# Kernel tuning notes

Hardware: AMD Instinct MI355X
Metric: run time of the kernel (lower is better)

The kernel has to match this reference:

```python
import jax, jax.numpy as jnp
import numpy as np

DIM = 128
N = 4096


def setup_inputs() -> dict:
    key = jax.random.key(0)
    ks = jax.random.split(key, 12)
    d = DIM
    s = 0.02
    inp = jax.random.normal(ks[0], (N, 2 * d), dtype=jnp.float32)
    # H = myLinear: (2d -> 5d -> 1), tanh after each layer
    Hw1 = jax.random.normal(ks[1], (2 * d, 5 * d), dtype=jnp.float32) * s
    Hb1 = jax.random.normal(ks[2], (5 * d,), dtype=jnp.float32) * s
    Hw2 = jax.random.normal(ks[3], (5 * d, 1), dtype=jnp.float32) * s
    Hb2 = jax.random.normal(ks[4], (1,), dtype=jnp.float32) * s
    # augment_f: (d -> 4d -> 8d -> d*d), tanh after each layer
    Aw1 = jax.random.normal(ks[5], (d, 4 * d), dtype=jnp.float32) * s
    Ab1 = jax.random.normal(ks[6], (4 * d,), dtype=jnp.float32) * s
    Aw2 = jax.random.normal(ks[7], (4 * d, 8 * d), dtype=jnp.float32) * s
    Ab2 = jax.random.normal(ks[8], (8 * d,), dtype=jnp.float32) * s
    Aw3 = jax.random.normal(ks[9], (8 * d, d * d), dtype=jnp.float32) * s
    Ab3 = jax.random.normal(ks[10], (d * d,), dtype=jnp.float32) * s
    u = jax.random.uniform(ks[11], (d,), dtype=jnp.float32, minval=-0.001, maxval=0.001)
    return {"t": 0, "inp": inp, "Hw1": Hw1, "Hb1": Hb1, "Hw2": Hw2, "Hb2": Hb2,
            "Aw1": Aw1, "Ab1": Ab1, "Aw2": Aw2, "Ab2": Ab2, "Aw3": Aw3, "Ab3": Ab3, "u": u}


def reference(t, inp, Hw1, Hb1, Hw2, Hb2, Aw1, Ab1, Aw2, Ab2, Aw3, Ab3, u):
    d = DIM
    n = inp.shape[0]

    def H_scalar(z):  # z: [2d] -> scalar
        h = jnp.tanh(z @ Hw1 + Hb1)
        return jnp.tanh(h @ Hw2 + Hb2)[0]

    # per-sample gradient of scalar H w.r.t. input (== batch_jacobian squeeze)
    g = jax.vmap(jax.grad(H_scalar))(inp)  # [N, 2d]
    dx = g[:, :d]
    dv = -g[:, d:]

    x = inp[:, :d]
    h1 = jnp.tanh(x @ Aw1 + Ab1)            # [N, 4d]
    h2 = jnp.tanh(h1 @ Aw2 + Ab2)           # [N, 8d]
    gq = jnp.tanh(h2 @ Aw3 + Ab3).reshape(n, d, d)  # [N, d, d]
    dv = dv + jnp.einsum("nij,j->ni", gq, u)
    return jnp.concatenate([dx, dv], axis=-1)  # [N, 2d]
```

## Files before the change

kernel.cpp:

```cpp
#include <hip/hip_runtime.h>
#include <hip/hip_bf16.h>
#include <cstdint>


typedef __bf16 bf16_t;
typedef __bf16 bf16x4_t __attribute__((ext_vector_type(4)));
typedef __bf16 bf16x8_t __attribute__((ext_vector_type(8)));
typedef float f32x4_t __attribute__((ext_vector_type(4)));
typedef float f32x16_t __attribute__((ext_vector_type(16)));
typedef int intx4_t __attribute__((ext_vector_type(4)));
typedef int intx8_t __attribute__((ext_vector_type(8)));

#define DIMD 128
#define NROW 4096
#define SMEM_G64 24576
#define SMEM3_BYTES 32768

__device__ __forceinline__ float fast_tanh(float x) {
  float t = __builtin_amdgcn_exp2f(x * 2.8853900817779268f);
  return 1.f - 2.f * __builtin_amdgcn_rcpf(t + 1.f);
}

__device__ __forceinline__ uint8_t to_fp8(float x) {
  return (uint8_t)(__builtin_amdgcn_cvt_pk_fp8_f32(x, x, 0, false) & 0xff);
}

__device__ __forceinline__ uint32_t pk4_fp8(float a, float b, float c,
                                            float d) {
  uint32_t lo = (uint32_t)__builtin_amdgcn_cvt_pk_fp8_f32(a, b, 0, false);
  return (uint32_t)__builtin_amdgcn_cvt_pk_fp8_f32(c, d, lo, true);
}

__device__ __forceinline__ void g2l16(const void* gp, void* lp) {
  __builtin_amdgcn_global_load_lds(
      reinterpret_cast<__attribute__((address_space(1))) void*>(
          reinterpret_cast<uintptr_t>(gp)),
      reinterpret_cast<__attribute__((address_space(3))) void*>(
          reinterpret_cast<uintptr_t>(lp)),
      16, 0, 0);
}

template <int CTRL>
__device__ __forceinline__ float dpp_addf(float v) {
  return v + __int_as_float(__builtin_amdgcn_update_dpp(
                 0, __float_as_int(v), CTRL, 0xf, 0xf, true));
}
__device__ __forceinline__ float dpp_sum32(float v) {
  v = dpp_addf<0x111>(v);
  v = dpp_addf<0x112>(v);
  v = dpp_addf<0x114>(v);
  v = dpp_addf<0x118>(v);
  v = dpp_addf<0x142>(v);
  return v;
}

template <int EPI>
__device__ __forceinline__ void gemm64_body(char* smem, int bx, int by,
                                            const bf16_t* A, int lda,
                                            const bf16_t* B, int ldb, int K,
                                            const float* bias, void* outp,
                                            int ldo) {
  constexpr int BK = 32;
  bf16_t* As = (bf16_t*)smem;
  bf16_t* Bs = As + 3 * 2048;
  const int NT = K / BK;

  const int m0 = bx * 64;
  const int n0 = by * 64;
  const int tid = threadIdx.x;
  const int wave = tid >> 6;
  const int lane = tid & 63;
  const int wm = wave >> 1;
  const int wn = wave & 1;

  const int sr = lane >> 2;
  const int sk = (((lane & 3) ^ ((sr >> 1) & 3)) * 8);
  const int fr = lane & 15;
  const int fk = (((lane >> 4) ^ ((fr >> 1) & 3)) * 8);
  const int rb = wave * 16;

  const bf16_t* Ag = A + (size_t)(m0 + rb + sr) * lda + sk;
  const bf16_t* Bg = B + (size_t)(n0 + rb + sr) * ldb + sk;

#define G64_STAGE(buf, k0)                              \
  do {                                                  \
    g2l16(Ag + (k0), As + (buf) * 2048 + rb * BK);      \
    g2l16(Bg + (k0), Bs + (buf) * 2048 + rb * BK);      \
  } while (0)

  f32x4_t acc[2][2] = {};

  G64_STAGE(0, 0);
  G64_STAGE(1, BK);
  asm volatile("s_waitcnt vmcnt(2)" ::: "memory");
  __builtin_amdgcn_s_barrier();
  asm volatile("" ::: "memory");

  for (int t = 0; t < NT; ++t) {
    if (t + 2 < NT) G64_STAGE((t + 2) % 3, (t + 2) * BK);
    const bf16_t* Ab = As + (t % 3) * 2048;
    const bf16_t* Bb = Bs + (t % 3) * 2048;

    bf16x8_t af[2], bb[2];
#pragma unroll
    for (int u = 0; u < 2; ++u) {
      af[u] = *(const bf16x8_t*)(Ab + (wm * 32 + u * 16 + fr) * BK + fk);
      bb[u] = *(const bf16x8_t*)(Bb + (wn * 32 + u * 16 + fr) * BK + fk);
    }
#pragma unroll
    for (int i = 0; i < 2; ++i)
#pragma unroll
      for (int j = 0; j < 2; ++j)
        acc[i][j] = __builtin_amdgcn_mfma_f32_16x16x32_bf16(af[i], bb[j],
                                                            acc[i][j], 0, 0, 0);
    if (t < NT - 1) {
      if (t + 2 < NT)
        asm volatile("s_waitcnt vmcnt(2)" ::: "memory");
      else
        asm volatile("s_waitcnt vmcnt(0)" ::: "memory");
      __builtin_amdgcn_s_barrier();
      asm volatile("" ::: "memory");
    }
  }
#undef G64_STAGE

#pragma unroll
  for (int i = 0; i < 2; ++i) {
    const int row = m0 + wm * 32 + i * 16 + (lane >> 4) * 4;
#pragma unroll
    for (int j = 0; j < 2; ++j) {
      const int col = n0 + wn * 32 + j * 16 + fr;
      if constexpr (EPI == 0) {
        bf16_t* O = (bf16_t*)outp;
        const float b = bias[col];
#pragma unroll
        for (int r = 0; r < 4; ++r)
          O[(size_t)(row + r) * ldo + col] = (bf16_t)fast_tanh(acc[i][j][r] + b);
      } else if constexpr (EPI == 1) {
        float* O = (float*)outp;
        const bool dx = (n0 < DIMD);
#pragma unroll
        for (int r = 0; r < 4; ++r) {
          const size_t idx = (size_t)(row + r) * ldo + col;
          if (dx) O[idx] = acc[i][j][r];
          else atomicAdd(&O[idx], -acc[i][j][r]);
        }
      } else {
        uint8_t* O = (uint8_t*)outp;
        const float b = bias[col];
#pragma unroll
        for (int r = 0; r < 4; ++r)
          O[(size_t)(row + r) * ldo + col] =
              to_fp8(64.f * fast_tanh(acc[i][j][r] + b));
      }
    }
  }
}

__device__ __forceinline__ void a3_body(char* smem, int bx, int by,
                                        const uint8_t* Arow,
                                        const uint8_t* BF, float* out,
                                        const float* ab3, const float* uvec) {
  constexpr int NT = 8;
  uint8_t* As = (uint8_t*)smem;

  const int tid = threadIdx.x;
  const int wave = tid >> 6;
  const int lane = tid & 63;
  const int wm = wave >> 1;
  const int wn = wave & 1;
  const int rl = lane & 31;
  const int c0 = lane >> 5;
  const int m0 = bx * 128;
  const int n0 = by * 128;

  const int sr = lane >> 2;
  const int sk = ((lane & 3) ^ ((sr >> 1) & 3)) * 16;
  const uint8_t* Ag = Arow + (size_t)(m0 + wave * 32 + sr) * 1024 + sk;
  const int lbase = wave * 2048;

#define A3_STAGE(buf, t)                                                     \
  do {                                                                       \
    _Pragma("unroll") for (int h_ = 0; h_ < 2; ++h_) {                       \
      g2l16(Ag + (size_t)(2 * (t) + h_) * 64,                                \
            As + (buf)*16384 + h_ * 8192 + lbase);                           \
      g2l16(Ag + 16 * 1024 + (size_t)(2 * (t) + h_) * 64,                    \
            As + (buf)*16384 + h_ * 8192 + lbase + 1024);                    \
    }                                                                        \
  } while (0)

  const uint8_t* Bg0 = BF + (size_t)(by * 4 + wn * 2 + 0) * 16 * 2048 + lane * 32;
  const uint8_t* Bg1 = BF + (size_t)(by * 4 + wn * 2 + 1) * 16 * 2048 + lane * 32;

  f32x16_t acc[2][2] = {};

  A3_STAGE(0, 0);
  asm volatile("s_waitcnt vmcnt(0)" ::: "memory");
  __builtin_amdgcn_s_barrier();
  asm volatile("" ::: "memory");

  const int w = (rl >> 1) & 3;
  const int sLo = ((2 * c0) ^ w) * 16;
  const int sHi = ((2 * c0 + 1) ^ w) * 16;

#pragma unroll
  for (int t = 0; t < NT; ++t) {
    if (t + 1 < NT) A3_STAGE((t + 1) & 1, t + 1);
    const uint8_t* Ab = As + (t & 1) * 16384;
#pragma unroll
    for (int kh = 0; kh < 2; ++kh) {
      const size_t ck = (size_t)(2 * t + kh) * 2048;
      intx8_t b0, b1;
      *(intx4_t*)&b0 = *(const intx4_t*)(Bg0 + ck);
      *((intx4_t*)&b0 + 1) = *(const intx4_t*)(Bg0 + ck + 16);
      *(intx4_t*)&b1 = *(const intx4_t*)(Bg1 + ck);
      *((intx4_t*)&b1 + 1) = *(const intx4_t*)(Bg1 + ck + 16);
#pragma unroll
      for (int i = 0; i < 2; ++i) {
        const int ra = (wm * 64 + i * 32 + rl) * 64;
        intx8_t af;
        *(intx4_t*)&af = *(const intx4_t*)(Ab + kh * 8192 + ra + sLo);
        *((intx4_t*)&af + 1) = *(const intx4_t*)(Ab + kh * 8192 + ra + sHi);
        acc[i][0] = __builtin_amdgcn_mfma_scale_f32_32x32x64_f8f6f4(
            af, b0, acc[i][0], 0, 0, 0, 0x79797979, 0, 0x79797979);
        acc[i][1] = __builtin_amdgcn_mfma_scale_f32_32x32x64_f8f6f4(
            af, b1, acc[i][1], 0, 0, 0, 0x79797979, 0, 0x79797979);
      }
    }
    if (t < NT - 1) {
      asm volatile("s_waitcnt vmcnt(0)" ::: "memory");
      __builtin_amdgcn_s_barrier();
      asm volatile("" ::: "memory");
    }
  }
#undef A3_STAGE

  const int q = lane >> 5;
  float uu[2], b3[2];
#pragma unroll
  for (int j = 0; j < 2; ++j) {
    uu[j] = uvec[wn * 64 + j * 32 + rl];
    b3[j] = ab3[n0 + wn * 64 + j * 32 + rl];
  }
  const int ocol = 128 + by;
#pragma unroll
  for (int i = 0; i < 2; ++i) {
    float s16[16];
#pragma unroll
    for (int r = 0; r < 16; ++r)
      s16[r] = fast_tanh(acc[i][0][r] + b3[0]) * uu[0] +
               fast_tanh(acc[i][1][r] + b3[1]) * uu[1];
#pragma unroll
    for (int r = 0; r < 16; ++r) s16[r] = dpp_sum32(s16[r]);
    if (rl == 31) {
      const int rowb = m0 + wm * 64 + i * 32 + 4 * q;
#pragma unroll
      for (int r = 0; r < 16; ++r)
        atomicAdd(&out[(size_t)(rowb + (r & 3) + 8 * (r >> 2)) * 256 + ocol],
                  s16[r]);
    }
  }
}

__device__ __forceinline__ void tcvt_body(char* smem, const float* in,
                                          bf16_t* out, int R, int C, int bx,
                                          int by) {
  float(*t)[33] = (float(*)[33])smem;
  const int c0 = bx * 32;
  const int r0 = by * 32;
  const int tx = threadIdx.x & 31;
  const int ty = threadIdx.x >> 5;
#pragma unroll
  for (int k = 0; k < 4; ++k)
    t[ty + k * 8][tx] = in[(size_t)(r0 + ty + k * 8) * C + c0 + tx];
  __syncthreads();
#pragma unroll
  for (int k = 0; k < 4; ++k)
    out[(size_t)(c0 + ty + k * 8) * R + r0 + tx] = (bf16_t)t[tx][ty + k * 8];
}

__device__ __forceinline__ void aw3t_body(char* smem, const float* Aw3,
                                          uint8_t* Aw3T8F, int b) {
  uint32_t(*T)[33] = (uint32_t(*)[33])smem;
  const int ct = b & 127;
  const int rt = b >> 7;
  const size_t c0 = (size_t)ct * 128;
  const int r0 = rt * 128;
  const int tx = threadIdx.x & 31;
  const int g = threadIdx.x >> 5;
#pragma unroll
  for (int k = 0; k < 4; ++k) {
    const int rr = r0 + 4 * g + 32 * k;
    const float4 v0 = *(const float4*)(Aw3 + (size_t)(rr + 0) * 16384 + c0 + 4 * tx);
    const float4 v1 = *(const float4*)(Aw3 + (size_t)(rr + 1) * 16384 + c0 + 4 * tx);
    const float4 v2 = *(const float4*)(Aw3 + (size_t)(rr + 2) * 16384 + c0 + 4 * tx);
    const float4 v3 = *(const float4*)(Aw3 + (size_t)(rr + 3) * 16384 + c0 + 4 * tx);
    const int r4 = g + 8 * k;
    T[4 * tx + 0][r4] = pk4_fp8(64.f * v0.x, 64.f * v1.x, 64.f * v2.x, 64.f * v3.x);
    T[4 * tx + 1][r4] = pk4_fp8(64.f * v0.y, 64.f * v1.y, 64.f * v2.y, 64.f * v3.y);
    T[4 * tx + 2][r4] = pk4_fp8(64.f * v0.z, 64.f * v1.z, 64.f * v2.z, 64.f * v3.z);
    T[4 * tx + 3][r4] = pk4_fp8(64.f * v0.w, 64.f * v1.w, 64.f * v2.w, 64.f * v3.w);
  }
  __syncthreads();
  const int kb = (rt << 1) + (tx >> 4);
  const int khalf = (tx >> 3) & 1;
  const int kin = (tx & 7) << 2;
#pragma unroll
  for (int k2 = 0; k2 < 16; ++k2) {
    const int cc = g + 8 * k2;
    const int cb = (ct << 2) + (cc >> 5);
    const int cin = cc & 31;
    *(uint32_t*)(Aw3T8F + (size_t)(cb * 16 + kb) * 2048 +
                 (khalf * 32 + cin) * 32 + kin) = T[cc][tx];
  }
}

__device__ __forceinline__ void hgrad_row(int row, const bf16_t* h,
                                          const float* Hw2, const float* Hb2,
                                          bf16_t* wout) {
  const int lane = threadIdx.x & 63;
  float hv[10], wv[10];
  float pre2 = 0.f;
#pragma unroll
  for (int t = 0; t < 10; ++t) {
    const int j = lane + t * 64;
    hv[t] = (float)h[(size_t)row * 640 + j];
    wv[t] = Hw2[j];
    pre2 += hv[t] * wv[t];
  }
#pragma unroll
  for (int d = 1; d < 64; d <<= 1) pre2 += __shfl_xor(pre2, d, 64);
  const float y = fast_tanh(pre2 + Hb2[0]);
  const float s = 1.f - y * y;
#pragma unroll
  for (int t = 0; t < 10; ++t) {
    const int j = lane + t * 64;
    wout[(size_t)row * 640 + j] = (bf16_t)(s * wv[t] * (1.f - hv[t] * hv[t]));
  }
}

__global__ __launch_bounds__(256) void launch0(
    const float* __restrict__ inp, bf16_t* __restrict__ inp_bf,
    const float* __restrict__ Hw1, bf16_t* __restrict__ Hw1T,
    bf16_t* __restrict__ Hw1_bf, const float* __restrict__ Aw1,
    bf16_t* __restrict__ Aw1T, const float* __restrict__ Aw2,
    bf16_t* __restrict__ Aw2T, float* __restrict__ out) {
  __shared__ __align__(16) char smem[4224];
  int b = blockIdx.x;
  if (b < 1024) {
    const int i = b * 256 + threadIdx.x;
    const float4 v = ((const float4*)inp)[i];
    bf16x4_t o = {(bf16_t)v.x, (bf16_t)v.y, (bf16_t)v.z, (bf16_t)v.w};
    ((bf16x4_t*)inp_bf)[i] = o;
  } else if (b < 1184) {
    int s = b - 1024;
    tcvt_body(smem, Hw1, Hw1T, 256, 640, s % 20, s / 20);
  } else if (b < 1248) {
    int s = b - 1184;
    tcvt_body(smem, Aw1, Aw1T, 128, 512, s % 16, s / 16);
  } else if (b < 1760) {
    int s = b - 1248;
    tcvt_body(smem, Aw2, Aw2T, 512, 1024, s % 32, s / 32);
  } else if (b < 1920) {
    const int i = (b - 1760) * 256 + threadIdx.x;
    const float4 v = ((const float4*)Hw1)[i];
    bf16x4_t o = {(bf16_t)v.x, (bf16_t)v.y, (bf16_t)v.z, (bf16_t)v.w};
    ((bf16x4_t*)Hw1_bf)[i] = o;
  } else {
    const int i = (b - 1920) * 256 + threadIdx.x;
    ((float4*)out)[i] = make_float4(0.f, 0.f, 0.f, 0.f);
  }
}

__global__ __launch_bounds__(256) void launch1(
    const bf16_t* __restrict__ inp_bf, const bf16_t* __restrict__ Hw1T,
    const float* __restrict__ Hb1, bf16_t* __restrict__ h_bf,
    const bf16_t* __restrict__ Aw1T, const float* __restrict__ Ab1,
    bf16_t* __restrict__ h1_bf, const float* __restrict__ Aw3,
    uint8_t* __restrict__ Aw3T8F) {
  __shared__ __align__(16) char smem[SMEM_G64];
  const int b = blockIdx.x;
  if (b < 640) {
    gemm64_body<0>(smem, b % 64, b / 64, inp_bf, 256, Hw1T, 256, 256, Hb1,
                   h_bf, 640);
  } else if (b < 1152) {
    const int i = b - 640;
    gemm64_body<0>(smem, i % 64, i / 64, inp_bf, 256, Aw1T, 128, 128, Ab1,
                   h1_bf, 512);
  } else {
    aw3t_body(smem, Aw3, Aw3T8F, b - 1152);
  }
}

__global__ __launch_bounds__(256) void launch2(
    const bf16_t* __restrict__ h1_bf, const bf16_t* __restrict__ Aw2T,
    const float* __restrict__ Ab2, uint8_t* __restrict__ h2_f8,
    const bf16_t* __restrict__ h_bf, const float* __restrict__ Hw2,
    const float* __restrict__ Hb2, bf16_t* __restrict__ w_bf,
    const float* __restrict__ Aw3, uint8_t* __restrict__ Aw3T8F) {
  __shared__ __align__(16) char smem[SMEM_G64];
  const int b = blockIdx.x;
  if (b < 1024) {
    gemm64_body<3>(smem, b % 64, b / 64, h1_bf, 512, Aw2T, 512, 512, Ab2,
                   h2_f8, 1024);
  } else if (b < 2048) {
    const int row = (b - 1024) * 4 + (threadIdx.x >> 6);
    hgrad_row(row, h_bf, Hw2, Hb2, w_bf);
  } else {
    aw3t_body(smem, Aw3, Aw3T8F, 512 + (b - 2048));
  }
}

__global__ __launch_bounds__(256, 4) void launch3(
    const bf16_t* __restrict__ w_bf, const bf16_t* __restrict__ Hw1_bf,
    float* __restrict__ out, const uint8_t* __restrict__ h2_f8,
    const uint8_t* __restrict__ Aw3T8F, const float* __restrict__ Ab3,
    const float* __restrict__ uvec) {
  __shared__ __align__(16) char smem[SMEM3_BYTES];
  const int b = blockIdx.x;
  if (b < 256) {
    gemm64_body<1>(smem, b % 64, b / 64, w_bf, 640, Hw1_bf, 640, 640, nullptr,
                   out, 256);
  } else {
    const int p = b - 256;
    const int by = (p & 7) * 16 + ((p >> 3) & 15);
    const int bx = p >> 7;
    a3_body(smem, bx, by, h2_f8, Aw3T8F, out, Ab3, uvec);
  }
}

extern "C" void kernel_launch(void* const* d_in, const int* in_sizes, int n_in,
                              void* d_out, int out_size, void* d_ws,
                              size_t ws_size, hipStream_t stream) {
  (void)in_sizes; (void)n_in; (void)out_size; (void)ws_size;
  const float* inp = (const float*)d_in[1];
  const float* Hw1 = (const float*)d_in[2];
  const float* Hb1 = (const float*)d_in[3];
  const float* Hw2 = (const float*)d_in[4];
  const float* Hb2 = (const float*)d_in[5];
  const float* Aw1 = (const float*)d_in[6];
  const float* Ab1 = (const float*)d_in[7];
  const float* Aw2 = (const float*)d_in[8];
  const float* Ab2 = (const float*)d_in[9];
  const float* Aw3 = (const float*)d_in[10];
  const float* Ab3 = (const float*)d_in[11];
  const float* u = (const float*)d_in[12];
  float* out = (float*)d_out;

  char* ws = (char*)d_ws;
  bf16_t* inp_bf = (bf16_t*)ws;    ws += (size_t)NROW * 256 * 2;
  bf16_t* Hw1_bf = (bf16_t*)ws;    ws += (size_t)256 * 640 * 2;
  bf16_t* Hw1T = (bf16_t*)ws;      ws += (size_t)640 * 256 * 2;
  bf16_t* Aw1T = (bf16_t*)ws;      ws += (size_t)512 * 128 * 2;
  bf16_t* Aw2T = (bf16_t*)ws;      ws += (size_t)1024 * 512 * 2;
  uint8_t* Aw3T8F = (uint8_t*)ws;  ws += (size_t)16384 * 1024;
  bf16_t* h_bf = (bf16_t*)ws;      ws += (size_t)NROW * 640 * 2;
  bf16_t* w_bf = (bf16_t*)ws;      ws += (size_t)NROW * 640 * 2;
  bf16_t* h1_bf = (bf16_t*)ws;     ws += (size_t)NROW * 512 * 2;
  uint8_t* h2_f8 = (uint8_t*)ws;   ws += (size_t)NROW * 1024;

  launch0<<<2944, 256, 0, stream>>>(inp, inp_bf, Hw1, Hw1T, Hw1_bf, Aw1, Aw1T,
                                    Aw2, Aw2T, out);
  launch1<<<1664, 256, 0, stream>>>(inp_bf, Hw1T, Hb1, h_bf, Aw1T, Ab1, h1_bf,
                                    Aw3, Aw3T8F);
  launch2<<<2560, 256, 0, stream>>>(h1_bf, Aw2T, Ab2, h2_f8, h_bf, Hw2, Hb2,
                                    w_bf, Aw3, Aw3T8F);
  launch3<<<4352, 256, 0, stream>>>(w_bf, Hw1_bf, out, h2_f8, Aw3T8F, Ab3, u);
}
```

Measured before the change: 226.0 us.

## Use 128x128 GEMM tiles for early layers and move Aw3 transpose to launch0

```diff
diff --git a/kernel.cpp b/kernel.cpp
--- a/kernel.cpp
+++ b/kernel.cpp
@@ -14,6 +14,8 @@
 #define DIMD 128
 #define NROW 4096
 #define SMEM_G64 24576
+#define SMEM_G128 49152
+#define SMEM_L0 16896
 #define SMEM3_BYTES 32768
 
 __device__ __forceinline__ float fast_tanh(float x) {
@@ -130,13 +132,7 @@
 #pragma unroll
     for (int j = 0; j < 2; ++j) {
       const int col = n0 + wn * 32 + j * 16 + fr;
-      if constexpr (EPI == 0) {
-        bf16_t* O = (bf16_t*)outp;
-        const float b = bias[col];
-#pragma unroll
-        for (int r = 0; r < 4; ++r)
-          O[(size_t)(row + r) * ldo + col] = (bf16_t)fast_tanh(acc[i][j][r] + b);
-      } else if constexpr (EPI == 1) {
+      if constexpr (EPI == 1) {
         float* O = (float*)outp;
         const bool dx = (n0 < DIMD);
 #pragma unroll
@@ -145,6 +141,101 @@
           if (dx) O[idx] = acc[i][j][r];
           else atomicAdd(&O[idx], -acc[i][j][r]);
         }
+      } else {
+        bf16_t* O = (bf16_t*)outp;
+        const float b = bias ? bias[col] : 0.f;
+#pragma unroll
+        for (int r = 0; r < 4; ++r)
+          O[(size_t)(row + r) * ldo + col] = (bf16_t)fast_tanh(acc[i][j][r] + b);
+      }
+    }
+  }
+}
+
+template <int EPI>
+__device__ __forceinline__ void gemm128_body(char* smem, int bx, int by,
+                                             const bf16_t* A, int lda,
+                                             const bf16_t* B, int ldb, int K,
+                                             const float* bias, void* outp,
+                                             int ldo) {
+  constexpr int BK = 32;
+  bf16_t* As = (bf16_t*)smem;
+  bf16_t* Bs = As + 3 * 4096;
+  const int NT = K / BK;
+
+  const int m0 = bx * 128;
+  const int n0 = by * 128;
+  const int tid = threadIdx.x;
+  const int wave = tid >> 6;
+  const int lane = tid & 63;
+  const int wm = wave >> 1;
+  const int wn = wave & 1;
+
+  const int sr = lane >> 2;
+  const int sk = (((lane & 3) ^ ((sr >> 1) & 3)) * 8);
+  const int fr = lane & 15;
+  const int fk = (((lane >> 4) ^ ((fr >> 1) & 3)) * 8);
+  const int rb = wave * 32;
+
+  const bf16_t* Ag = A + (size_t)(m0 + rb + sr) * lda + sk;
+  const bf16_t* Bg = B + (size_t)(n0 + rb + sr) * ldb + sk;
+
+#define G128_STAGE(buf, k0)                                                  \
+  do {                                                                       \
+    g2l16(Ag + (k0), As + (buf) * 4096 + rb * BK);                           \
+    g2l16(Ag + (size_t)16 * lda + (k0), As + (buf) * 4096 + (rb + 16) * BK); \
+    g2l16(Bg + (k0), Bs + (buf) * 4096 + rb * BK);                           \
+    g2l16(Bg + (size_t)16 * ldb + (k0), Bs + (buf) * 4096 + (rb + 16) * BK); \
+  } while (0)
+
+  f32x4_t acc[4][4] = {};
+
+  G128_STAGE(0, 0);
+  G128_STAGE(1, BK);
+  asm volatile("s_waitcnt vmcnt(4)" ::: "memory");
+  __builtin_amdgcn_s_barrier();
+  asm volatile("" ::: "memory");
+
+  for (int t = 0; t < NT; ++t) {
+    if (t + 2 < NT) G128_STAGE((t + 2) % 3, (t + 2) * BK);
+    const bf16_t* Ab = As + (t % 3) * 4096;
+    const bf16_t* Bb = Bs + (t % 3) * 4096;
+
+    bf16x8_t af[4], bb[4];
+#pragma unroll
+    for (int u = 0; u < 4; ++u) {
+      af[u] = *(const bf16x8_t*)(Ab + (wm * 64 + u * 16 + fr) * BK + fk);
+      bb[u] = *(const bf16x8_t*)(Bb + (wn * 64 + u * 16 + fr) * BK + fk);
+    }
+#pragma unroll
+    for (int i = 0; i < 4; ++i)
+#pragma unroll
+      for (int j = 0; j < 4; ++j)
+        acc[i][j] = __builtin_amdgcn_mfma_f32_16x16x32_bf16(af[i], bb[j],
+                                                            acc[i][j], 0, 0, 0);
+    if (t < NT - 1) {
+      if (t + 2 < NT)
+        asm volatile("s_waitcnt vmcnt(4)" ::: "memory");
+      else
+        asm volatile("s_waitcnt vmcnt(0)" ::: "memory");
+      __builtin_amdgcn_s_barrier();
+      asm volatile("" ::: "memory");
+    }
+  }
+#undef G128_STAGE
+
+#pragma unroll
+  for (int i = 0; i < 4; ++i) {
+    const int row = m0 + wm * 64 + i * 16 + (lane >> 4) * 4;
+#pragma unroll
+    for (int j = 0; j < 4; ++j) {
+      const int col = n0 + wn * 64 + j * 16 + fr;
+      if constexpr (EPI == 0) {
+        bf16_t* O = (bf16_t*)outp;
+        const float b = bias[col];
+#pragma unroll
+        for (int r = 0; r < 4; ++r)
+          O[(size_t)(row + r) * ldo + col] = (bf16_t)fast_tanh(acc[i][j][r] + b);
       } else {
         uint8_t* O = (uint8_t*)outp;
         const float b = bias[col];
@@ -344,8 +435,9 @@
     const float* __restrict__ Hw1, bf16_t* __restrict__ Hw1T,
     bf16_t* __restrict__ Hw1_bf, const float* __restrict__ Aw1,
     bf16_t* __restrict__ Aw1T, const float* __restrict__ Aw2,
-    bf16_t* __restrict__ Aw2T, float* __restrict__ out) {
-  __shared__ __align__(16) char smem[4224];
+    bf16_t* __restrict__ Aw2T, float* __restrict__ out,
+    const float* __restrict__ Aw3, uint8_t* __restrict__ Aw3T8F) {
+  __shared__ __align__(16) char smem[SMEM_L0];
   int b = blockIdx.x;
   if (b < 1024) {
     const int i = b * 256 + threadIdx.x;
@@ -366,48 +458,44 @@
     const float4 v = ((const float4*)Hw1)[i];
     bf16x4_t o = {(bf16_t)v.x, (bf16_t)v.y, (bf16_t)v.z, (bf16_t)v.w};
     ((bf16x4_t*)Hw1_bf)[i] = o;
-  } else {
+  } else if (b < 2944) {
     const int i = (b - 1920) * 256 + threadIdx.x;
     ((float4*)out)[i] = make_float4(0.f, 0.f, 0.f, 0.f);
-  }
-}
-
-__global__ __launch_bounds__(256) void launch1(
+  } else {
+    aw3t_body(smem, Aw3, Aw3T8F, b - 2944);
+  }
+}
+
+__global__ __launch_bounds__(256, 3) void launch1(
     const bf16_t* __restrict__ inp_bf, const bf16_t* __restrict__ Hw1T,
     const float* __restrict__ Hb1, bf16_t* __restrict__ h_bf,
     const bf16_t* __restrict__ Aw1T, const float* __restrict__ Ab1,
-    bf16_t* __restrict__ h1_bf, const float* __restrict__ Aw3,
-    uint8_t* __restrict__ Aw3T8F) {
-  __shared__ __align__(16) char smem[SMEM_G64];
+    bf16_t* __restrict__ h1_bf) {
+  __shared__ __align__(16) char smem[SMEM_G128];
   const int b = blockIdx.x;
-  if (b < 640) {
-    gemm64_body<0>(smem, b % 64, b / 64, inp_bf, 256, Hw1T, 256, 256, Hb1,
-                   h_bf, 640);
-  } else if (b < 1152) {
-    const int i = b - 640;
-    gemm64_body<0>(smem, i % 64, i / 64, inp_bf, 256, Aw1T, 128, 128, Ab1,
-                   h1_bf, 512);
+  if (b < 160) {
+    gemm128_body<0>(smem, b % 32, b / 32, inp_bf, 256, Hw1T, 256, 256, Hb1,
+                    h_bf, 640);
   } else {
-    aw3t_body(smem, Aw3, Aw3T8F, b - 1152);
-  }
-}
-
-__global__ __launch_bounds__(256) void launch2(
+    const int i = b - 160;
+    gemm128_body<0>(smem, i % 32, i / 32, inp_bf, 256, Aw1T, 128, 128, Ab1,
+                    h1_bf, 512);
+  }
+}
+
+__global__ __launch_bounds__(256, 3) void launch2(
     const bf16_t* __restrict__ h1_bf, const bf16_t* __restrict__ Aw2T,
     const float* __restrict__ Ab2, uint8_t* __restrict__ h2_f8,
     const bf16_t* __restrict__ h_bf, const float* __restrict__ Hw2,
-    const float* __restrict__ Hb2, bf16_t* __restrict__ w_bf,
-    const float* __restrict__ Aw3, uint8_t* __restrict__ Aw3T8F) {
-  __shared__ __align__(16) char smem[SMEM_G64];
+    const float* __restrict__ Hb2, bf16_t* __restrict__ w_bf) {
+  __shared__ __align__(16) char smem[SMEM_G128];
   const int b = blockIdx.x;
-  if (b < 1024) {
-    gemm64_body<3>(smem, b % 64, b / 64, h1_bf, 512, Aw2T, 512, 512, Ab2,
-                   h2_f8, 1024);
-  } else if (b < 2048) {
-    const int row = (b - 1024) * 4 + (threadIdx.x >> 6);
+  if (b < 256) {
+    gemm128_body<3>(smem, b % 32, b / 32, h1_bf, 512, Aw2T, 512, 512, Ab2,
+                    h2_f8, 1024);
+  } else {
+    const int row = (b - 256) * 4 + (threadIdx.x >> 6);
     hgrad_row(row, h_bf, Hw2, Hb2, w_bf);
-  } else {
-    aw3t_body(smem, Aw3, Aw3T8F, 512 + (b - 2048));
   }
 }
 
@@ -459,11 +547,10 @@
   bf16_t* h1_bf = (bf16_t*)ws;     ws += (size_t)NROW * 512 * 2;
   uint8_t* h2_f8 = (uint8_t*)ws;   ws += (size_t)NROW * 1024;
 
-  launch0<<<2944, 256, 0, stream>>>(inp, inp_bf, Hw1, Hw1T, Hw1_bf, Aw1, Aw1T,
-                                    Aw2, Aw2T, out);
-  launch1<<<1664, 256, 0, stream>>>(inp_bf, Hw1T, Hb1, h_bf, Aw1T, Ab1, h1_bf,
-                                    Aw3, Aw3T8F);
-  launch2<<<2560, 256, 0, stream>>>(h1_bf, Aw2T, Ab2, h2_f8, h_bf, Hw2, Hb2,
-                                    w_bf, Aw3, Aw3T8F);
+  launch0<<<3968, 256, 0, stream>>>(inp, inp_bf, Hw1, Hw1T, Hw1_bf, Aw1, Aw1T,
+                                    Aw2, Aw2T, out, Aw3, Aw3T8F);
+  launch1<<<288, 256, 0, stream>>>(inp_bf, Hw1T, Hb1, h_bf, Aw1T, Ab1, h1_bf);
+  launch2<<<1280, 256, 0, stream>>>(h1_bf, Aw2T, Ab2, h2_f8, h_bf, Hw2, Hb2,
+                                    w_bf);
   launch3<<<4352, 256, 0, stream>>>(w_bf, Hw1_bf, out, h2_f8, Aw3T8F, Ab3, u);
 }
```

Measured after the change: 229.4 us. Within noise of the previous version (+1.5%).
